# Performance work log

Measured on AMD Instinct MI355X. Metric: run time of the kernel, lower is better.

The kernel has to match this reference:

```python
import jax, jax.numpy as jnp
import numpy as np

NEG = -1e30  # log-space 'zero'
BLANK = 0


def setup_inputs() -> dict:
    key = jax.random.key(0)
    k1, k2, k3, k4, k5, k6 = jax.random.split(key, 6)
    B, T, D, V, L = 16, 500, 256, 5000, 50
    encoder_out = jax.random.normal(k1, (B, T, D), dtype=jnp.float32)
    encoder_out_lens = jax.random.randint(k2, (B,), 400, T + 1, dtype=jnp.int32)
    y = jax.random.randint(k3, (B, L), 1, V, dtype=jnp.int32)  # blank=0 excluded
    y_lens = jax.random.randint(k4, (B,), 30, L + 1, dtype=jnp.int32)
    W = jax.random.normal(k5, (V, D), dtype=jnp.float32) * (1.0 / np.sqrt(D))
    b = jax.random.normal(k6, (V,), dtype=jnp.float32) * 0.01
    return {"encoder_out": encoder_out, "encoder_out_lens": encoder_out_lens,
            "y": y, "y_lens": y_lens, "W": W, "b": b}


def _ctc_neg_logp(lp, ext, skip, enc_lens, y_lens):
    # lp: [T,B,V] log-probs; ext: [B,S] extended label seq (blank interleaved)
    T, B, V = lp.shape
    S = ext.shape[1]
    # per-frame log-probs of the extended labels: [T,B,S]
    lp_ext = jnp.take_along_axis(lp, jnp.broadcast_to(ext[None], (T, B, S)), axis=2)

    end_idx = jnp.stack([2 * y_lens, 2 * y_lens - 1], axis=1)  # [B,2]

    def end_of(alpha):
        vals = jnp.take_along_axis(alpha, end_idx, axis=1)  # [B,2]
        return jnp.logaddexp(vals[:, 0], vals[:, 1])

    alpha0 = jnp.full((B, S), NEG, lp.dtype)
    alpha0 = alpha0.at[:, 0].set(lp_ext[0, :, 0])
    alpha0 = alpha0.at[:, 1].set(lp_ext[0, :, 1])

    pad1 = jnp.full((B, 1), NEG, lp.dtype)
    pad2 = jnp.full((B, 2), NEG, lp.dtype)

    def step(alpha, lp_t):
        prev1 = jnp.concatenate([pad1, alpha[:, :-1]], axis=1)
        prev2 = jnp.concatenate([pad2, alpha[:, :-2]], axis=1)
        m = jnp.logaddexp(alpha, prev1)
        m = jnp.logaddexp(m, jnp.where(skip, prev2, NEG))
        new = m + lp_t
        return new, end_of(new)

    _, ends_rest = jax.lax.scan(step, alpha0, lp_ext[1:])  # [T-1,B]
    ends = jnp.concatenate([end_of(alpha0)[None], ends_rest], axis=0)  # [T,B]
    final = jnp.take_along_axis(ends, (enc_lens - 1)[None, :], axis=0)[0]  # [B]
    return -final


def reference(encoder_out, encoder_out_lens, y, y_lens, W, b):
    # dropout is identity here (deterministic/eval reference)
    B = encoder_out.shape[0]
    logits = jnp.einsum('btd,vd->btv', encoder_out, W) + b  # [B,T,V]
    lp = jax.nn.log_softmax(logits, axis=-1)
    lp = jnp.transpose(lp, (1, 0, 2))  # [T,B,V]

    L = y.shape[1]
    S = 2 * L + 1
    ext = jnp.zeros((B, S), dtype=y.dtype).at[:, 1::2].set(y)  # blank-interleaved
    s_idx = jnp.arange(S)
    ext_m2 = jnp.concatenate([jnp.zeros((B, 2), ext.dtype), ext[:, :-2]], axis=1)
    skip = (s_idx[None, :] >= 2) & (ext != ext_m2) & (ext != BLANK)

    neg_logp = _ctc_neg_logp(lp, ext, skip, encoder_out_lens, y_lens)
    loss = jnp.sum(neg_logp) / B  # CTCLoss(reduction='sum') / batch_size
    return loss
```

## Files before the change

### kernel.cpp

```cpp
#include <hip/hip_runtime.h>
#include <hip/hip_bf16.h>

#define NEG (-1e30f)
#define M_ROWS 8000
#define N_COLS 5000
#define K_DIM  256
#define T_LEN  500
#define T_PAD  512
#define B_SZ   16
#define L_LAB  50
#define DP_STR  516
#define LOG2E   1.4426950408889634f
#define LN2     0.6931471805599453f

typedef _Float16 half8  __attribute__((ext_vector_type(8)));
typedef _Float16 half4v __attribute__((ext_vector_type(4)));
typedef float    floatx4 __attribute__((ext_vector_type(4)));

__device__ __forceinline__ float fexp2(float x) {
#if defined(__has_builtin)
#if __has_builtin(__builtin_amdgcn_exp2f)
  return __builtin_amdgcn_exp2f(x);
#else
  return __expf(x * LN2);
#endif
#else
  return __expf(x * LN2);
#endif
}
__device__ __forceinline__ float flog2(float x) {
#if defined(__has_builtin)
#if __has_builtin(__builtin_amdgcn_logf)
  return __builtin_amdgcn_logf(x);
#else
  return __logf(x) * LOG2E;
#endif
#else
  return __logf(x) * LOG2E;
#endif
}
__device__ __forceinline__ float wave_shr1(float x, float fill) {
#if defined(__has_builtin)
#if __has_builtin(__builtin_amdgcn_update_dpp)
  int r = __builtin_amdgcn_update_dpp(__float_as_int(fill), __float_as_int(x),
                                      0x138 , 0xf, 0xf, false);
  return __int_as_float(r);
#else
  return __shfl_up(x, 1);
#endif
#else
  return __shfl_up(x, 1);
#endif
}

__device__ __forceinline__ void gload_lds16(const _Float16* g, _Float16* l) {
  __builtin_amdgcn_global_load_lds(
      (const __attribute__((address_space(1))) void*)g,
      (__attribute__((address_space(3))) void*)l,
      16, 0, 0);
}

__global__ void k_f2h2(const float* __restrict__ enc, const float* __restrict__ W,
                       _Float16* __restrict__ ench, _Float16* __restrict__ wh,
                       float* z, float* psum) {
  int i = blockIdx.x * blockDim.x + threadIdx.x;
  if (i == 0) z[0] = 0.0f;
  if (i < M_ROWS) psum[i] = 0.0f;
  if (i < 512000) {
    float4 v = ((const float4*)enc)[i];
    half4v o = {(_Float16)v.x, (_Float16)v.y, (_Float16)v.z, (_Float16)v.w};
    ((half4v*)ench)[i] = o;
  } else {
    int k = i - 512000;
    if (k < 320000) {
      float4 v = ((const float4*)W)[k];
      half4v o = {(_Float16)v.x, (_Float16)v.y, (_Float16)v.z, (_Float16)v.w};
      ((half4v*)wh)[k] = o;
    }
  }
}

__global__ __launch_bounds__(256) void k_gemm_lse(
    const _Float16* __restrict__ A, const _Float16* __restrict__ Bm,
    const float* __restrict__ bias, const int* __restrict__ y,
    float* __restrict__ psum, float* __restrict__ lgT) {
  __shared__ _Float16 As[128 * 64];
  __shared__ _Float16 Bs[128 * 64];

  const int tid = threadIdx.x;
  const int lane = tid & 63;
  const int wid = tid >> 6;
  const int wave_m = wid & 1, wave_n = wid >> 1;
  const int l15 = lane & 15, quad = lane >> 4;

  const int flat = blockIdx.x;
  const int wg = (flat & 7) * 315 + (flat >> 3);
  const int n0 = (wg % 40) * 128;
  const int m0 = (wg / 40) * 128;

  floatx4 acc[4][4];
  floatx4 zz = {0.f, 0.f, 0.f, 0.f};
  #pragma unroll
  for (int mi = 0; mi < 4; ++mi)
    #pragma unroll
    for (int ni = 0; ni < 4; ++ni) acc[mi][ni] = zz;

  const int lrow = lane >> 3;
  const int co = (((lane & 7) ^ lrow) * 8);
  const int rsw = (l15 & 7) << 3;

  #pragma unroll
  for (int kk = 0; kk < K_DIM; kk += 64) {
    #pragma unroll
    for (int q = 0; q < 4; ++q) {
      const int r = wid * 32 + q * 8 + lrow;
      int ga = m0 + r; if (ga > M_ROWS - 1) ga = M_ROWS - 1;
      int gb = n0 + r; if (gb > N_COLS - 1) gb = N_COLS - 1;
      gload_lds16(A + (size_t)ga * K_DIM + kk + co, As + (wid * 32 + q * 8) * 64);
      gload_lds16(Bm + (size_t)gb * K_DIM + kk + co, Bs + (wid * 32 + q * 8) * 64);
    }
    __syncthreads();
    #pragma unroll
    for (int ko = 0; ko < 64; ko += 32) {
      half8 af[4], bf[4];
      #pragma unroll
      for (int mi = 0; mi < 4; ++mi)
        af[mi] = *(const half8*)(As + (wave_m * 64 + mi * 16 + l15) * 64 + ((ko + quad * 8) ^ rsw));
      #pragma unroll
      for (int ni = 0; ni < 4; ++ni)
        bf[ni] = *(const half8*)(Bs + (wave_n * 64 + ni * 16 + l15) * 64 + ((ko + quad * 8) ^ rsw));
      #pragma unroll
      for (int mi = 0; mi < 4; ++mi)
        #pragma unroll
        for (int ni = 0; ni < 4; ++ni)
          acc[mi][ni] = __builtin_amdgcn_mfma_f32_16x16x32_f16(af[mi], bf[ni], acc[mi][ni], 0, 0, 0);
    }
    __syncthreads();
  }

  float bvv[4]; bool cok[4];
  #pragma unroll
  for (int ni = 0; ni < 4; ++ni) {
    int col = n0 + wave_n * 64 + ni * 16 + l15;
    cok[ni] = (col < N_COLS);
    bvv[ni] = cok[ni] ? bias[col] : 0.f;
  }

  const int nbase = n0 + wave_n * 64;
  const int mbase = m0 + wave_m * 64;
  int b_lo = mbase / T_LEN;
  int b_hi = (mbase + 63) / T_LEN;
  if (b_hi > B_SZ - 1) b_hi = B_SZ - 1;
  for (int b = b_lo; b <= b_hi; ++b) {
    int v_l = 0x40000000;
    if (lane <= 50) v_l = (lane == 0) ? 0 : y[b * L_LAB + lane - 1];
    int dv_l = v_l - nbase;
    unsigned long long mask = __ballot(dv_l >= 0 && dv_l < 64);
    while (mask) {
      int j = (int)__builtin_ctzll(mask);
      mask &= mask - 1;
      int dv = __shfl(dv_l, j);
      int ni = dv >> 4;
      float bb = bvv[0];
      bb = (ni == 1) ? bvv[1] : bb;
      bb = (ni == 2) ? bvv[2] : bb;
      bb = (ni == 3) ? bvv[3] : bb;
      if ((dv & 15) == l15) {
        #pragma unroll
        for (int mi = 0; mi < 4; ++mi) {
          #pragma unroll
          for (int r = 0; r < 4; ++r) {
            float val = acc[mi][0][r];
            val = (ni == 1) ? acc[mi][1][r] : val;
            val = (ni == 2) ? acc[mi][2][r] : val;
            val = (ni == 3) ? acc[mi][3][r] : val;
            int grow = mbase + mi * 16 + quad * 4 + r;
            int t = grow - b * T_LEN;
            if (t >= 0 && t < T_LEN && grow < M_ROWS)
              lgT[((size_t)b * 51 + j) * T_PAD + t] = val + bb;
          }
        }
      }
    }
  }

  #pragma unroll
  for (int mi = 0; mi < 4; ++mi) {
    #pragma unroll
    for (int r = 0; r < 4; ++r) {
      int grow = mbase + mi * 16 + quad * 4 + r;
      float se = 0.f;
      se += cok[0] ? fexp2((acc[mi][0][r] + bvv[0]) * LOG2E) : 0.f;
      se += cok[1] ? fexp2((acc[mi][1][r] + bvv[1]) * LOG2E) : 0.f;
      se += cok[2] ? fexp2((acc[mi][2][r] + bvv[2]) * LOG2E) : 0.f;
      se += cok[3] ? fexp2((acc[mi][3][r] + bvv[3]) * LOG2E) : 0.f;
      #pragma unroll
      for (int d = 1; d < 16; d <<= 1) se += __shfl_xor(se, d);
      if (l15 == 0 && grow < M_ROWS) atomicAdd(&psum[grow], se);
    }
  }
}

__global__ __launch_bounds__(256) void k_dp(
    const float* __restrict__ lgT, const float* __restrict__ psum,
    const int* __restrict__ enc_lens, const int* __restrict__ y,
    const int* __restrict__ y_lens, float* __restrict__ out) {
  __shared__ float sA[51 * DP_STR];
  __shared__ float sRed[5];
  const int b = blockIdx.x, tid = threadIdx.x;
  const int Tb = enc_lens[b], yl = y_lens[b];

  const float* g = lgT + (size_t)b * 51 * T_PAD;
  #pragma unroll
  for (int k = 0; k < 26; ++k) {
    int idx = tid + k * 256;
    if (idx < 51 * 128) {
      int row = idx >> 7, c4 = (idx & 127) << 2;
      float4 v = *(const float4*)(g + (size_t)row * T_PAD + c4);
      float4 s = {v.x * LOG2E, v.y * LOG2E, v.z * LOG2E, v.w * LOG2E};
      *(float4*)(sA + row * DP_STR + c4) = s;
    }
  }

  float sl2 = 0.f;
  for (int t = tid; t < Tb; t += 256) sl2 += flog2(psum[b * T_LEN + t]);
  #pragma unroll
  for (int d = 1; d < 64; d <<= 1) sl2 += __shfl_xor(sl2, d);
  if ((tid & 63) == 0) sRed[1 + (tid >> 6)] = sl2;
  __syncthreads();
  const float slse = LN2 * (sRed[1] + sRed[2] + sRed[3] + sRed[4]);

  if (tid < 64) {
    const int i = tid;
    const int jj = (i + 1 < 50) ? (i + 1) : 50;
    const float* bl = sA;
    const float* ow = sA + jj * DP_STR;
    const bool v0 = (i <= 50), v1 = (i <= 49);
    const bool lane0 = (i == 0);
    const bool skip1 = (i >= 1 && i <= 49) && (y[b * L_LAB + i] != y[b * L_LAB + i - 1]);

    float4 A0 = *(const float4*)(bl + 0),  A1 = *(const float4*)(ow + 0);
    float4 B0 = *(const float4*)(bl + 4),  B1 = *(const float4*)(ow + 4);
    float4 C0 = *(const float4*)(bl + 8),  C1 = *(const float4*)(ow + 8);
    float4 D0 = *(const float4*)(bl + 12), D1 = *(const float4*)(ow + 12);
    const float4 n4 = {NEG, NEG, NEG, NEG};
    if (!v1) { A1 = n4; B1 = n4; C1 = n4; D1 = n4; }

    float a0 = lane0 ? A0.x : NEG;
    float a1 = lane0 ? A1.x : NEG;

    auto step = [&](float l0r, float l1) {
      float l0 = v0 ? l0r : NEG;
      float p1 = wave_shr1(a1, NEG);
      p1 = lane0 ? NEG : p1;
      float th = skip1 ? p1 : NEG;
      float m0 = fmaxf(a0, p1);
      float na0 = m0 + flog2(fexp2(a0 - m0) + fexp2(p1 - m0)) + l0;
      float m1 = fmaxf(fmaxf(a1, a0), th);
      float na1 = m1 + flog2(fexp2(a1 - m1) + fexp2(a0 - m1) + fexp2(th - m1)) + l1;
      a0 = na0; a1 = na1;
    };

    step(A0.y, A1.y);
    step(A0.z, A1.z);
    step(A0.w, A1.w);

    float4 c0 = B0, c1 = B1, n0v = C0, n1v = C1, nn0 = D0, nn1 = D1;
    int t = 4;
    while (t + 4 <= Tb) {
      float4 p0 = *(const float4*)(bl + t + 12);
      float4 p1v = *(const float4*)(ow + t + 12);
      if (!v1) p1v = n4;
      step(c0.x, c1.x);
      step(c0.y, c1.y);
      step(c0.z, c1.z);
      step(c0.w, c1.w);
      c0 = n0v; c1 = n1v; n0v = nn0; n1v = nn1; nn0 = p0; nn1 = p1v;
      t += 4;
    }
    if (t < Tb) { step(c0.x, c1.x); ++t; }
    if (t < Tb) { step(c0.y, c1.y); ++t; }
    if (t < Tb) { step(c0.z, c1.z); ++t; }

    float ea = __shfl(a0, yl);
    float eb = __shfl(a1, yl - 1);
    if (lane0) {
      float m = fmaxf(ea, eb);
      float fin = LN2 * (m + flog2(fexp2(ea - m) + fexp2(eb - m)));
      atomicAdd(out, (slse - fin) * (1.0f / (float)B_SZ));
    }
  }
}

extern "C" void kernel_launch(void* const* d_in, const int* in_sizes, int n_in,
                              void* d_out, int out_size, void* d_ws, size_t ws_size,
                              hipStream_t stream) {
  (void)in_sizes; (void)n_in; (void)out_size; (void)ws_size;
  const float* enc      = (const float*)d_in[0];
  const int*   enc_lens = (const int*)d_in[1];
  const int*   y        = (const int*)d_in[2];
  const int*   y_lens   = (const int*)d_in[3];
  const float* W        = (const float*)d_in[4];
  const float* bias     = (const float*)d_in[5];
  float* out = (float*)d_out;

  char* ws = (char*)d_ws;
  _Float16* ench = (_Float16*)(ws + 0);
  _Float16* wh   = (_Float16*)(ws + 4096000);
  float* psum    = (float*)(ws + 6656000);
  float* lgT     = (float*)(ws + 6688000);

  k_f2h2<<<3250, 256, 0, stream>>>(enc, W, ench, wh, out, psum);
  k_gemm_lse<<<2520, 256, 0, stream>>>(ench, wh, bias, y, psum, lgT);
  k_dp<<<16, 256, 0, stream>>>(lgT, psum, enc_lens, y, y_lens, out);
}
```

Baseline: 180.1 us.

## Double-buffer LDS tiles in GEMM-LSE kernel with async prefetch

```diff
diff --git a/kernel.cpp b/kernel.cpp
--- a/kernel.cpp
+++ b/kernel.cpp
@@ -84,8 +84,8 @@
     const _Float16* __restrict__ A, const _Float16* __restrict__ Bm,
     const float* __restrict__ bias, const int* __restrict__ y,
     float* __restrict__ psum, float* __restrict__ lgT) {
-  __shared__ _Float16 As[128 * 64];
-  __shared__ _Float16 Bs[128 * 64];
+  __shared__ _Float16 As[2 * 128 * 64];
+  __shared__ _Float16 Bs[2 * 128 * 64];
 
   const int tid = threadIdx.x;
   const int lane = tid & 63;
@@ -109,33 +109,59 @@
   const int co = (((lane & 7) ^ lrow) * 8);
   const int rsw = (l15 & 7) << 3;
 
-  #pragma unroll
-  for (int kk = 0; kk < K_DIM; kk += 64) {
+  auto stage = [&](int kk, int buf) {
     #pragma unroll
     for (int q = 0; q < 4; ++q) {
       const int r = wid * 32 + q * 8 + lrow;
       int ga = m0 + r; if (ga > M_ROWS - 1) ga = M_ROWS - 1;
       int gb = n0 + r; if (gb > N_COLS - 1) gb = N_COLS - 1;
-      gload_lds16(A + (size_t)ga * K_DIM + kk + co, As + (wid * 32 + q * 8) * 64);
-      gload_lds16(Bm + (size_t)gb * K_DIM + kk + co, Bs + (wid * 32 + q * 8) * 64);
-    }
-    __syncthreads();
-    #pragma unroll
-    for (int ko = 0; ko < 64; ko += 32) {
-      half8 af[4], bf[4];
-      #pragma unroll
-      for (int mi = 0; mi < 4; ++mi)
-        af[mi] = *(const half8*)(As + (wave_m * 64 + mi * 16 + l15) * 64 + ((ko + quad * 8) ^ rsw));
+      gload_lds16(A + (size_t)ga * K_DIM + kk * 64 + co, As + buf * 8192 + (wid * 32 + q * 8) * 64);
+      gload_lds16(Bm + (size_t)gb * K_DIM + kk * 64 + co, Bs + buf * 8192 + (wid * 32 + q * 8) * 64);
+    }
+  };
+
+  stage(0, 0);
+  stage(1, 1);
+
+  #pragma unroll
+  for (int kk = 0; kk < 4; ++kk) {
+    const int cur = kk & 1;
+    if (kk < 3) asm volatile("s_waitcnt vmcnt(8)" ::: "memory");
+    else        asm volatile("s_waitcnt vmcnt(0)" ::: "memory");
+    __builtin_amdgcn_s_barrier();
+
+    half8 af[4], bf[4];
+    #pragma unroll
+    for (int mi = 0; mi < 4; ++mi)
+      af[mi] = *(const half8*)(As + cur * 8192 + (wave_m * 64 + mi * 16 + l15) * 64 + ((0 + quad * 8) ^ rsw));
+    #pragma unroll
+    for (int ni = 0; ni < 4; ++ni)
+      bf[ni] = *(const half8*)(Bs + cur * 8192 + (wave_n * 64 + ni * 16 + l15) * 64 + ((0 + quad * 8) ^ rsw));
+    asm volatile("s_waitcnt lgkmcnt(0)" ::: "memory");
+    __builtin_amdgcn_sched_barrier(0);
+    #pragma unroll
+    for (int mi = 0; mi < 4; ++mi)
       #pragma unroll
       for (int ni = 0; ni < 4; ++ni)
-        bf[ni] = *(const half8*)(Bs + (wave_n * 64 + ni * 16 + l15) * 64 + ((ko + quad * 8) ^ rsw));
+        acc[mi][ni] = __builtin_amdgcn_mfma_f32_16x16x32_f16(af[mi], bf[ni], acc[mi][ni], 0, 0, 0);
+
+    half8 ag[4], bg[4];
+    #pragma unroll
+    for (int mi = 0; mi < 4; ++mi)
+      ag[mi] = *(const half8*)(As + cur * 8192 + (wave_m * 64 + mi * 16 + l15) * 64 + ((32 + quad * 8) ^ rsw));
+    #pragma unroll
+    for (int ni = 0; ni < 4; ++ni)
+      bg[ni] = *(const half8*)(Bs + cur * 8192 + (wave_n * 64 + ni * 16 + l15) * 64 + ((32 + quad * 8) ^ rsw));
+    asm volatile("s_waitcnt lgkmcnt(0)" ::: "memory");
+    __builtin_amdgcn_sched_barrier(0);
+    __builtin_amdgcn_s_barrier();
+    if (kk < 2) stage(kk + 2, cur);
+
+    #pragma unroll
+    for (int mi = 0; mi < 4; ++mi)
       #pragma unroll
-      for (int mi = 0; mi < 4; ++mi)
-        #pragma unroll
-        for (int ni = 0; ni < 4; ++ni)
-          acc[mi][ni] = __builtin_amdgcn_mfma_f32_16x16x32_f16(af[mi], bf[ni], acc[mi][ni], 0, 0, 0);
-    }
-    __syncthreads();
+      for (int ni = 0; ni < 4; ++ni)
+        acc[mi][ni] = __builtin_amdgcn_mfma_f32_16x16x32_f16(ag[mi], bg[ni], acc[mi][ni], 0, 0, 0);
   }
 
   float bvv[4]; bool cok[4];
```

After: 179.1 us. Within noise of the previous version (-0.6%).
